# Performance work log

Measured on AMD Instinct MI355X. Metric: run time of the kernel, lower is better.

The kernel has to match this reference:

```python
import jax, jax.numpy as jnp
import numpy as np

NEG_INF = -jnp.inf


def setup_inputs() -> dict:
    key = jax.random.key(0)
    ks = jax.random.split(key, 8)
    B, Lq, Lk, D, H = 8, 2048, 2048, 256, 128
    queries = jax.random.normal(ks[0], (B, Lq, D), dtype=jnp.float32)
    keys = jax.random.normal(ks[1], (B, Lk, D), dtype=jnp.float32)
    values_1 = jax.random.normal(ks[2], (B, Lk, D), dtype=jnp.float32)
    values_2 = jax.random.normal(ks[3], (B, Lq, D), dtype=jnp.float32)
    values_1_mask = jax.random.randint(ks[4], (B, Lk), 0, 2).astype(bool)
    values_2_mask = jax.random.randint(ks[5], (B, Lq), 0, 2).astype(bool)
    # xavier_normal for Linear(D -> H): std = sqrt(2/(D+H))
    std = float(np.sqrt(2.0 / (D + H)))
    Wq = jax.random.normal(ks[6], (H, D), dtype=jnp.float32) * std
    Wk = jax.random.normal(ks[7], (H, D), dtype=jnp.float32) * std
    scaling = jnp.ones((1, H), dtype=jnp.float32)
    return {
        "queries": queries, "keys": keys,
        "values_1": values_1, "values_1_mask": values_1_mask,
        "values_2": values_2, "values_2_mask": values_2_mask,
        "Wq": Wq, "Wk": Wk, "scaling": scaling,
    }


def reference(queries, keys, values_1, values_1_mask, values_2, values_2_mask, Wq, Wk, scaling):
    # projections + relu (eval mode: dropout inactive)
    pq = jax.nn.relu(jnp.einsum("bqd,hd->bqh", queries, Wq))        # [B,Lq,H]
    pk = jax.nn.relu(jnp.einsum("bkd,hd->bkh", keys, Wk)) * scaling  # [B,Lk,H]
    scores = jnp.einsum("bqh,bkh->bqk", pq, pk)                      # [B,Lq,Lk]

    # branch 2: softmax over queries axis of scores^T, masked by values_2_mask [B,Lq]
    scores_T = jnp.where(values_2_mask[:, None, :], NEG_INF, jnp.swapaxes(scores, 1, 2))  # [B,Lk,Lq]
    alpha_2 = jax.nn.softmax(scores_T, axis=2)
    output_2 = jnp.einsum("bkq,bqd->bkd", alpha_2, values_2)         # [B,Lk,D]

    # branch 1: softmax over keys axis, masked by values_1_mask [B,Lk]
    scores_1 = jnp.where(values_1_mask[:, None, :], NEG_INF, scores)  # [B,Lq,Lk]
    alpha_1 = jax.nn.softmax(scores_1, axis=2)
    output = jnp.einsum("bqk,bkd->bqd", alpha_1, values_1)           # [B,Lq,D]

    return (output, output_2)
```

## Files before the change

kernel.cpp:

```cpp
#include <hip/hip_runtime.h>
#include <cstdint>
#include <math.h>

#define B 8
#define L 2048
#define D 256
#define H 128

typedef __attribute__((ext_vector_type(8))) _Float16 half8;
typedef __attribute__((ext_vector_type(4))) _Float16 half4t;
typedef __attribute__((ext_vector_type(4))) float f32x4;
typedef unsigned short ushort;
typedef unsigned int uint;


__global__ void prep_kernel(const void* __restrict__ raw0,
                            const void* __restrict__ raw1,
                            const float* __restrict__ Wq,
                            const float* __restrict__ Wk,
                            float* __restrict__ fb1,
                            float* __restrict__ fb2,
                            _Float16* __restrict__ Wf) {
    const int t = threadIdx.x;
    const int z = blockIdx.y;
    {
        const void* raw = z ? raw1 : raw0;
        float* outb = z ? fb2 : fb1;
        const uint* wd = (const uint*)raw;
        __shared__ int flag;
        if (t == 0) flag = 0;
        __syncthreads();
        if (wd[t] > 1u) flag = 1;
        __syncthreads();
        const int base = blockIdx.x * 1024;
        if (flag) {
            const uint8_t* by = (const uint8_t*)raw;
#pragma unroll
            for (int j = 0; j < 4; ++j) {
                int i = base + t + 256 * j;
                outb[i] = by[i] ? -INFINITY : 0.f;
            }
        } else {
#pragma unroll
            for (int j = 0; j < 4; ++j) {
                int i = base + t + 256 * j;
                outb[i] = wd[i] ? -INFINITY : 0.f;
            }
        }
    }
    {
        const float* Wsrc = z ? Wk : Wq;
        const int chunk = blockIdx.x * 256 + t;
        const int h = chunk >> 5;
        const int d0 = (chunk & 31) * 8;
        float4 v0 = *(const float4*)(Wsrc + (size_t)h * 256 + d0);
        float4 v1 = *(const float4*)(Wsrc + (size_t)h * 256 + d0 + 4);
        half8 hv;
        hv[0] = (_Float16)v0.x; hv[1] = (_Float16)v0.y;
        hv[2] = (_Float16)v0.z; hv[3] = (_Float16)v0.w;
        hv[4] = (_Float16)v1.x; hv[5] = (_Float16)v1.y;
        hv[6] = (_Float16)v1.z; hv[7] = (_Float16)v1.w;
        const int db = d0 >> 5, dq = (d0 >> 3) & 3;
        size_t off = (size_t)z * 32768 +
                     ((size_t)((h >> 4) * 8 + db)) * 512 + dq * 128 + (h & 15) * 8;
        *(half8*)(Wf + off) = hv;
    }
}

__launch_bounds__(256, 2)
__global__ void proj_mfma_kernel(const float* __restrict__ queries,
                                 const float* __restrict__ keys,
                                 const _Float16* __restrict__ Wf,
                                 const float* __restrict__ scaling,
                                 _Float16* __restrict__ pqo,
                                 _Float16* __restrict__ pko) {
    const int t = threadIdx.x;
    const int w = t >> 6;
    const int lane = t & 63;
    const int l15 = lane & 15;
    const int quad = lane >> 4;
    const int z = blockIdx.z;
    const int half = blockIdx.y;
    const int r0 = blockIdx.x * 64;
    const float* in = z ? keys : queries;
    _Float16* outp = z ? pko : pqo;

    __shared__ __attribute__((aligned(16))) _Float16 Wl[32 * 512];
    __shared__ __attribute__((aligned(16))) _Float16 Af[4][8 * 512];

    {
        const _Float16* wsrc = Wf + ((size_t)z * 64 + half * 32) * 512;
#pragma unroll
        for (int i = 0; i < 8; ++i) {
            const int f = w * 8 + i;
            __builtin_amdgcn_global_load_lds(
                (const __attribute__((address_space(1))) uint*)(wsrc + f * 512 + lane * 8),
                (__attribute__((address_space(3))) uint*)(Wl + f * 512 + lane * 8),
                16, 0, 0);
        }
    }
    {
#pragma unroll
        for (int j = 0; j < 16; ++j) {
            const int idx = t + 256 * j;
            const int row = idx >> 6;
            const int c4 = idx & 63;
            float4 v = *(const float4*)(in + ((size_t)(r0 + row)) * 256 + c4 * 4);
            half4t h4;
            h4[0] = (_Float16)v.x; h4[1] = (_Float16)v.y;
            h4[2] = (_Float16)v.z; h4[3] = (_Float16)v.w;
            const int rt = row >> 4, rl = row & 15;
            const int d0 = c4 * 4;
            const int db = d0 >> 5, dq = (d0 >> 3) & 3, e = d0 & 7;
            *(half4t*)(&Af[rt][db * 512 + dq * 128 + rl * 8 + e]) = h4;
        }
    }
    __syncthreads();

    half8 a[8];
#pragma unroll
    for (int db = 0; db < 8; ++db)
        a[db] = *(const half8*)(&Af[w][db * 512 + lane * 8]);

    f32x4 acc[4];
#pragma unroll
    for (int hti = 0; hti < 4; ++hti) acc[hti] = (f32x4){0.f, 0.f, 0.f, 0.f};
#pragma unroll
    for (int db = 0; db < 8; ++db)
#pragma unroll
        for (int hti = 0; hti < 4; ++hti) {
            half8 bfrag = *(const half8*)(Wl + (hti * 8 + db) * 512 + lane * 8);
            acc[hti] = __builtin_amdgcn_mfma_f32_16x16x32_f16(a[db], bfrag, acc[hti], 0, 0, 0);
        }

    _Float16* S = Af[w];
#pragma unroll
    for (int hti = 0; hti < 4; ++hti) {
        const int hl_ = hti * 16 + l15;
        const int hb = hl_ >> 5, hq = (hl_ >> 3) & 3, e = hl_ & 7;
        const float scl = z ? scaling[half * 64 + hl_] : 1.f;
#pragma unroll
        for (int r = 0; r < 4; ++r) {
            float v = fmaxf(acc[hti][r], 0.f) * scl;
            S[hb * 512 + hq * 128 + (quad * 4 + r) * 8 + e] = (_Float16)v;
        }
    }
    const size_t grow16 = (size_t)(r0 >> 4) + w;
    _Float16* gout = outp + (grow16 * 4 + half * 2) * 512;
#pragma unroll
    for (int hb = 0; hb < 2; ++hb) {
        half8 vv = *(const half8*)(S + hb * 512 + lane * 8);
        *(half8*)(gout + hb * 512 + lane * 8) = vv;
    }
}

__global__ void vtrans_kernel(const float* __restrict__ v1,
                              const float* __restrict__ v2,
                              _Float16* __restrict__ vt1,
                              _Float16* __restrict__ vt2) {
    const int t = threadIdx.x;
    const int zz = blockIdx.z;
    const int b = zz & 7;
    const int which = zz >> 3;
    const float* src = (which ? v2 : v1) + (size_t)b * L * D;
    _Float16* dst = which ? vt2 : vt1;
    const int k0 = blockIdx.x * 64;
    const int d0 = blockIdx.y * 64;
    __shared__ float lt[64][65];
#pragma unroll
    for (int p = 0; p < 4; ++p) {
        int kr = p * 16 + (t >> 4);
        float4 v = *(const float4*)(src + (size_t)(k0 + kr) * D + d0 + (t & 15) * 4);
        lt[(t & 15) * 4 + 0][kr] = v.x;
        lt[(t & 15) * 4 + 1][kr] = v.y;
        lt[(t & 15) * 4 + 2][kr] = v.z;
        lt[(t & 15) * 4 + 3][kr] = v.w;
    }
    __syncthreads();
    const int d = t & 63;
    const int kk = (t >> 6) & 1;
    const int qp = t >> 7;
    const size_t tile = ((size_t)b * L + k0) / 32 + kk;
    const int ct = (d0 + d) >> 4;
    _Float16* base = dst + (tile * 16 + ct) * 512 + (d & 15) * 8;
#pragma unroll
    for (int s = 0; s < 2; ++s) {
        const int qv = qp * 2 + s;
        const float* lr = &lt[d][kk * 32 + qv * 8];
        half8 hv;
#pragma unroll
        for (int e = 0; e < 8; ++e) hv[e] = (_Float16)lr[e];
        *(half8*)(base + qv * 128) = hv;
    }
}

__launch_bounds__(256, 3)
__global__ void flash_mfma_kernel(const _Float16* __restrict__ pq,
                                  const _Float16* __restrict__ pk,
                                  const float* __restrict__ fb1,
                                  const float* __restrict__ fb2,
                                  const _Float16* __restrict__ vt1,
                                  const _Float16* __restrict__ vt2,
                                  float* __restrict__ out) {
    const int t = threadIdx.x;
    const int w = t >> 6;
    const int lane = t & 63;
    const int l15 = lane & 15;
    const int quad = lane >> 4;
    const int bb = blockIdx.y;
    const int q0 = blockIdx.x * 64 + w * 16;

    const _Float16 *Qp, *Kp, *Vp;
    const float* fb;
    float* O;
    if (blockIdx.z == 0) { Qp = pq; Kp = pk; fb = fb1; Vp = vt1; O = out; }
    else                 { Qp = pk; Kp = pq; fb = fb2; Vp = vt2; O = out + (size_t)B * L * D; }

    __shared__ __attribute__((aligned(16))) _Float16 kv[2][24 * 512];
    __shared__ __attribute__((aligned(16))) _Float16 Pl[4][16][40];

    const size_t bL = (size_t)bb * L;

    half8 aq[4];
    {
        const _Float16* qb = Qp + (size_t)((bL + q0) >> 4) * 2048 + lane * 8;
#pragma unroll
        for (int hb = 0; hb < 4; ++hb) aq[hb] = *(const half8*)(qb + hb * 512);
    }

    f32x4 acc[16];
#pragma unroll
    for (int ct = 0; ct < 16; ++ct) acc[ct] = (f32x4){0.f, 0.f, 0.f, 0.f};
    float m_run[4], l_run[4];
#pragma unroll
    for (int r = 0; r < 4; ++r) { m_run[r] = -INFINITY; l_run[r] = 0.f; }

    auto stage = [&](int tile, int buf) {
        const size_t kk0 = bL + (size_t)tile * 32;
        _Float16* lb = kv[buf];
#pragma unroll
        for (int i = 0; i < 6; ++i) {
            const int c = w * 6 + i;
            const _Float16* g;
            if (c < 8)
                g = Kp + (size_t)(((kk0 >> 4) + (c >> 2)) * 4 + (c & 3)) * 512;
            else
                g = Vp + (size_t)((kk0 >> 5) * 16 + (c - 8)) * 512;
            __builtin_amdgcn_global_load_lds(
                (const __attribute__((address_space(1))) uint*)(g + lane * 8),
                (__attribute__((address_space(3))) uint*)(lb + c * 512),
                16, 0, 0);
        }
    };

    stage(0, 0);
    float nb0 = fb[bL + l15];
    float nb1 = fb[bL + 16 + l15];

    for (int it = 0; it < L / 32; ++it) {
        const int buf = it & 1;
        __syncthreads();
        if (it + 1 < L / 32) stage(it + 1, buf ^ 1);
        const float bias0 = nb0, bias1 = nb1;
        if (it + 1 < L / 32) {
            nb0 = fb[bL + (it + 1) * 32 + l15];
            nb1 = fb[bL + (it + 1) * 32 + 16 + l15];
        }

        const _Float16* kb = kv[buf];

        f32x4 s[2];
#pragma unroll
        for (int jt = 0; jt < 2; ++jt) {
            f32x4 sv = (f32x4){0.f, 0.f, 0.f, 0.f};
#pragma unroll
            for (int hb = 0; hb < 4; ++hb) {
                half8 bk = *(const half8*)(kb + (jt * 4 + hb) * 512 + lane * 8);
                sv = __builtin_amdgcn_mfma_f32_16x16x32_f16(aq[hb], bk, sv, 0, 0, 0);
            }
            s[jt] = sv;
        }
#pragma unroll
        for (int r = 0; r < 4; ++r) { s[0][r] += bias0; s[1][r] += bias1; }

        float al[4];
#pragma unroll
        for (int r = 0; r < 4; ++r) {
            float tm = fmaxf(s[0][r], s[1][r]);
            tm = fmaxf(tm, __shfl_xor(tm, 1));
            tm = fmaxf(tm, __shfl_xor(tm, 2));
            tm = fmaxf(tm, __shfl_xor(tm, 4));
            tm = fmaxf(tm, __shfl_xor(tm, 8));
            const float mn = fmaxf(m_run[r], tm);
            const float alpha = (m_run[r] == -INFINITY) ? 0.f : __expf(m_run[r] - mn);
            const float safe = (mn == -INFINITY) ? 0.f : mn;
            _Float16 p0 = (_Float16)__expf(s[0][r] - safe);
            _Float16 p1 = (_Float16)__expf(s[1][r] - safe);
            Pl[w][quad * 4 + r][l15] = p0;
            Pl[w][quad * 4 + r][16 + l15] = p1;
            float ps = (float)p0 + (float)p1;
            ps += __shfl_xor(ps, 1);
            ps += __shfl_xor(ps, 2);
            ps += __shfl_xor(ps, 4);
            ps += __shfl_xor(ps, 8);
            m_run[r] = mn;
            l_run[r] = l_run[r] * alpha + ps;
            al[r] = alpha;
        }

        const bool need = (al[0] != 1.f) | (al[1] != 1.f) | (al[2] != 1.f) | (al[3] != 1.f);
        if (__any(need)) {
#pragma unroll
            for (int ct = 0; ct < 16; ++ct)
#pragma unroll
                for (int r = 0; r < 4; ++r) acc[ct][r] *= al[r];
        }

        half8 pa = *(const half8*)&Pl[w][l15][quad * 8];
#pragma unroll
        for (int ct = 0; ct < 16; ++ct) {
            half8 bv = *(const half8*)(kb + (8 + ct) * 512 + lane * 8);
            acc[ct] = __builtin_amdgcn_mfma_f32_16x16x32_f16(pa, bv, acc[ct], 0, 0, 0);
        }
    }

    float inv[4];
#pragma unroll
    for (int r = 0; r < 4; ++r)
        inv[r] = (l_run[r] > 0.f) ? (1.f / l_run[r]) : 0.f;
#pragma unroll
    for (int r = 0; r < 4; ++r) {
        float* orow = O + (bL + q0 + quad * 4 + r) * (size_t)D + l15;
#pragma unroll
        for (int ct = 0; ct < 16; ++ct)
            orow[ct * 16] = acc[ct][r] * inv[r];
    }
}

extern "C" void kernel_launch(void* const* d_in, const int* in_sizes, int n_in,
                              void* d_out, int out_size, void* d_ws, size_t ws_size,
                              hipStream_t stream) {
    const float* queries  = (const float*)d_in[0];
    const float* keys     = (const float*)d_in[1];
    const float* values_1 = (const float*)d_in[2];
    const void*  v1_mask  = d_in[3];
    const float* values_2 = (const float*)d_in[4];
    const void*  v2_mask  = d_in[5];
    const float* Wq       = (const float*)d_in[6];
    const float* Wk       = (const float*)d_in[7];
    const float* scaling  = (const float*)d_in[8];
    float* out = (float*)d_out;

    _Float16* pqw = (_Float16*)d_ws;
    _Float16* pkw = pqw + (size_t)B * L * H;
    _Float16* vt1 = pkw + (size_t)B * L * H;
    _Float16* vt2 = vt1 + (size_t)B * L * D;
    float* fb1 = (float*)(vt2 + (size_t)B * L * D);
    float* fb2 = fb1 + B * L;
    _Float16* Wf = (_Float16*)(fb2 + B * L);

    prep_kernel<<<dim3(16, 2), 256, 0, stream>>>(
        v1_mask, v2_mask, Wq, Wk, fb1, fb2, Wf);
    proj_mfma_kernel<<<dim3(B * L / 64, 2, 2), 256, 0, stream>>>(
        queries, keys, Wf, scaling, pqw, pkw);
    vtrans_kernel<<<dim3(L / 64, D / 64, B * 2), 256, 0, stream>>>(
        values_1, values_2, vt1, vt2);
    flash_mfma_kernel<<<dim3(L / 64, B, 2), 256, 0, stream>>>(
        pqw, pkw, fb1, fb2, vt1, vt2, out);
}
```

Baseline: 256.0 us.

## Compute scores once, share them across both softmax branches with precomputed row maxima

Replaces the fused flash kernel, which computed QK^T twice (once per branch), with a score kernel that computes each score tile once. It stores the tile in fp16 relative to a per-tile max and records per-row and per-column tile maxima. A second kernel reduces these maxima into exact row maxes up front, then exponentiates the stored scores and runs the PV MFMA without online rescaling. This halves the QK matmul work and removes the running-max correction, but adds a 64 MB fp16 score buffer written and read through global memory. The transposed branch also reads scores through LDS with strided accesses.

```diff
diff --git a/kernel.cpp b/kernel.cpp
--- a/kernel.cpp
+++ b/kernel.cpp
@@ -194,146 +194,237 @@
     }
 }
 
+__launch_bounds__(256)
+__global__ void score_kernel(const _Float16* __restrict__ pq,
+                             const _Float16* __restrict__ pk,
+                             const float* __restrict__ fb1,
+                             const float* __restrict__ fb2,
+                             _Float16* __restrict__ Sb,
+                             float* __restrict__ tmax1,
+                             float* __restrict__ tmax2,
+                             float* __restrict__ mmax) {
+    const int t = threadIdx.x;
+    const int w = t >> 6;
+    const int lane = t & 63;
+    const int l15 = lane & 15;
+    const int quad = lane >> 4;
+    const int bb = blockIdx.z;
+    const int k0 = blockIdx.x * 64;
+    const int q0 = blockIdx.y * 64;
+    const size_t bL = (size_t)bb * L;
+    const int qt16 = (q0 >> 4) + w;
+
+    half8 aq[4];
+    {
+        const _Float16* qb = pq + ((bL + q0 + w * 16) >> 4) * 2048 + lane * 8;
+#pragma unroll
+        for (int hb = 0; hb < 4; ++hb) aq[hb] = *(const half8*)(qb + hb * 512);
+    }
+
+    f32x4 s[4];
+#pragma unroll
+    for (int jt = 0; jt < 4; ++jt) {
+        const _Float16* kb = pk + ((bL + k0 + jt * 16) >> 4) * 2048 + lane * 8;
+        f32x4 sv = (f32x4){0.f, 0.f, 0.f, 0.f};
+#pragma unroll
+        for (int hb = 0; hb < 4; ++hb) {
+            half8 bk = *(const half8*)(kb + hb * 512);
+            sv = __builtin_amdgcn_mfma_f32_16x16x32_f16(aq[hb], bk, sv, 0, 0, 0);
+        }
+        s[jt] = sv;
+    }
+
+    float b1j[4];
+#pragma unroll
+    for (int jt = 0; jt < 4; ++jt) b1j[jt] = fb1[bL + k0 + jt * 16 + l15];
+    float4 b2v = *(const float4*)(fb2 + bL + q0 + w * 16 + quad * 4);
+    float b2r[4] = {b2v.x, b2v.y, b2v.z, b2v.w};
+
+#pragma unroll
+    for (int r = 0; r < 4; ++r) {
+        float m1 = -INFINITY;
+#pragma unroll
+        for (int jt = 0; jt < 4; ++jt) m1 = fmaxf(m1, s[jt][r] + b1j[jt]);
+        m1 = fmaxf(m1, __shfl_xor(m1, 1));
+        m1 = fmaxf(m1, __shfl_xor(m1, 2));
+        m1 = fmaxf(m1, __shfl_xor(m1, 4));
+        m1 = fmaxf(m1, __shfl_xor(m1, 8));
+        if (l15 == 0)
+            tmax1[(bL + q0 + w * 16 + quad * 4 + r) * 32 + blockIdx.x] = m1;
+    }
+
+#pragma unroll
+    for (int jt = 0; jt < 4; ++jt) {
+        float m2 = -INFINITY, mm = -INFINITY;
+#pragma unroll
+        for (int r = 0; r < 4; ++r) {
+            m2 = fmaxf(m2, s[jt][r] + b2r[r]);
+            mm = fmaxf(mm, s[jt][r]);
+        }
+        m2 = fmaxf(m2, __shfl_xor(m2, 16));
+        m2 = fmaxf(m2, __shfl_xor(m2, 32));
+        if (quad == 0)
+            tmax2[(bL + k0 + jt * 16 + l15) * 128 + qt16] = m2;
+        mm = fmaxf(mm, __shfl_xor(mm, 1));
+        mm = fmaxf(mm, __shfl_xor(mm, 2));
+        mm = fmaxf(mm, __shfl_xor(mm, 4));
+        mm = fmaxf(mm, __shfl_xor(mm, 8));
+        mm = fmaxf(mm, __shfl_xor(mm, 16));
+        mm = fmaxf(mm, __shfl_xor(mm, 32));
+        const size_t mti = ((size_t)bb * 128 + qt16) * 128 + (k0 >> 4) + jt;
+        if (lane == 0) mmax[mti] = mm;
+        _Float16* sp = Sb + mti * 256 + l15;
+#pragma unroll
+        for (int r = 0; r < 4; ++r)
+            sp[(quad * 4 + r) * 16] = (_Float16)(s[jt][r] - mm);
+    }
+}
+
 __launch_bounds__(256, 3)
-__global__ void flash_mfma_kernel(const _Float16* __restrict__ pq,
-                                  const _Float16* __restrict__ pk,
-                                  const float* __restrict__ fb1,
-                                  const float* __restrict__ fb2,
-                                  const _Float16* __restrict__ vt1,
-                                  const _Float16* __restrict__ vt2,
-                                  float* __restrict__ out) {
+__global__ void attn_pv_kernel(const _Float16* __restrict__ Sb,
+                               const float* __restrict__ fb1,
+                               const float* __restrict__ fb2,
+                               const float* __restrict__ tmax1,
+                               const float* __restrict__ tmax2,
+                               const float* __restrict__ mmax,
+                               const _Float16* __restrict__ vt1,
+                               const _Float16* __restrict__ vt2,
+                               float* __restrict__ out) {
     const int t = threadIdx.x;
     const int w = t >> 6;
     const int lane = t & 63;
     const int l15 = lane & 15;
     const int quad = lane >> 4;
     const int bb = blockIdx.y;
-    const int q0 = blockIdx.x * 64 + w * 16;
-
-    const _Float16 *Qp, *Kp, *Vp;
-    const float* fb;
-    float* O;
-    if (blockIdx.z == 0) { Qp = pq; Kp = pk; fb = fb1; Vp = vt1; O = out; }
-    else                 { Qp = pk; Kp = pq; fb = fb2; Vp = vt2; O = out + (size_t)B * L * D; }
-
-    __shared__ __attribute__((aligned(16))) _Float16 kv[2][24 * 512];
-    __shared__ __attribute__((aligned(16))) _Float16 Pl[4][16][40];
-
+    const int z = blockIdx.z;
+    const int r0 = blockIdx.x * 64;
     const size_t bL = (size_t)bb * L;
 
-    half8 aq[4];
-    {
-        const _Float16* qb = Qp + (size_t)((bL + q0) >> 4) * 2048 + lane * 8;
-#pragma unroll
-        for (int hb = 0; hb < 4; ++hb) aq[hb] = *(const half8*)(qb + hb * 512);
+    const _Float16* Vp = z ? vt2 : vt1;
+    const float* fbb = (z ? fb2 : fb1) + bL;
+    float* O = out + (z ? (size_t)B * L * D : 0);
+
+    __shared__ __attribute__((aligned(16))) _Float16 kv[2][16 * 512];
+    __shared__ __attribute__((aligned(16))) _Float16 sst[2][4 * 1056];
+    __shared__ float mred[64][4];
+
+    {
+        const int row = t >> 2, part = t & 3;
+        float mv = -INFINITY;
+        if (z == 0) {
+            const float4* p4 = (const float4*)(tmax1 + ((bL + r0 + row) << 5)) + part * 2;
+#pragma unroll
+            for (int i = 0; i < 2; ++i) {
+                float4 v = p4[i];
+                mv = fmaxf(mv, fmaxf(fmaxf(v.x, v.y), fmaxf(v.z, v.w)));
+            }
+        } else {
+            const float4* p4 = (const float4*)(tmax2 + ((bL + r0 + row) << 7)) + part * 8;
+#pragma unroll
+            for (int i = 0; i < 8; ++i) {
+                float4 v = p4[i];
+                mv = fmaxf(mv, fmaxf(fmaxf(v.x, v.y), fmaxf(v.z, v.w)));
+            }
+        }
+        mred[row][part] = mv;
+    }
+
+    auto stage = [&](int it, int buf) {
+        const _Float16* vb = Vp + ((bL + it * 32) >> 5) * (size_t)(16 * 512);
+#pragma unroll
+        for (int i = 0; i < 4; ++i) {
+            const int c = w * 4 + i;
+            __builtin_amdgcn_global_load_lds(
+                (const __attribute__((address_space(1))) uint*)(vb + c * 512 + lane * 8),
+                (__attribute__((address_space(3))) uint*)(&kv[buf][c * 512] + lane * 8),
+                16, 0, 0);
+        }
+        if (z) {
+            const _Float16* ssrc = Sb +
+                (((size_t)bb * 128 + it * 2 + (w >> 1)) * 128 + (r0 >> 4) + (w & 1) * 2) * 256;
+            __builtin_amdgcn_global_load_lds(
+                (const __attribute__((address_space(1))) uint*)(ssrc + lane * 8),
+                (__attribute__((address_space(3))) uint*)(&sst[buf][w * 1056] + lane * 8),
+                16, 0, 0);
+        }
+    };
+
+    stage(0, 0);
+    __syncthreads();
+
+    float mreg;
+    {
+        const int row = w * 16 + l15;
+        mreg = fmaxf(fmaxf(mred[row][0], mred[row][1]),
+                     fmaxf(mred[row][2], mred[row][3]));
+        mreg = fmaxf(mreg, -1e30f);
     }
 
     f32x4 acc[16];
 #pragma unroll
     for (int ct = 0; ct < 16; ++ct) acc[ct] = (f32x4){0.f, 0.f, 0.f, 0.f};
-    float m_run[4], l_run[4];
-#pragma unroll
-    for (int r = 0; r < 4; ++r) { m_run[r] = -INFINITY; l_run[r] = 0.f; }
-
-    auto stage = [&](int tile, int buf) {
-        const size_t kk0 = bL + (size_t)tile * 32;
-        _Float16* lb = kv[buf];
-#pragma unroll
-        for (int i = 0; i < 6; ++i) {
-            const int c = w * 6 + i;
-            const _Float16* g;
-            if (c < 8)
-                g = Kp + (size_t)(((kk0 >> 4) + (c >> 2)) * 4 + (c & 3)) * 512;
-            else
-                g = Vp + (size_t)((kk0 >> 5) * 16 + (c - 8)) * 512;
-            __builtin_amdgcn_global_load_lds(
-                (const __attribute__((address_space(1))) uint*)(g + lane * 8),
-                (__attribute__((address_space(3))) uint*)(lb + c * 512),
-                16, 0, 0);
-        }
-    };
-
-    stage(0, 0);
-    float nb0 = fb[bL + l15];
-    float nb1 = fb[bL + 16 + l15];
-
-    for (int it = 0; it < L / 32; ++it) {
+    float lsum = 0.f;
+
+    for (int it = 0; it < 64; ++it) {
         const int buf = it & 1;
-        __syncthreads();
-        if (it + 1 < L / 32) stage(it + 1, buf ^ 1);
-        const float bias0 = nb0, bias1 = nb1;
-        if (it + 1 < L / 32) {
-            nb0 = fb[bL + (it + 1) * 32 + l15];
-            nb1 = fb[bL + (it + 1) * 32 + 16 + l15];
-        }
-
+        if (it) __syncthreads();
+        if (it + 1 < 64) stage(it + 1, buf ^ 1);
+
+        float c;
+        {
+            const size_t mmidx = z
+                ? (((size_t)bb * 128 + it * 2 + (quad >> 1)) * 128 + (r0 >> 4) + w)
+                : (((size_t)bb * 128 + (r0 >> 4) + w) * 128 + it * 2 + (quad >> 1));
+            c = mmax[mmidx] - mreg;
+        }
+        float bj[8];
+        {
+            const float4* bp = (const float4*)(fbb + it * 32 + quad * 8);
+            float4 b0 = bp[0], b1 = bp[1];
+            bj[0] = b0.x; bj[1] = b0.y; bj[2] = b0.z; bj[3] = b0.w;
+            bj[4] = b1.x; bj[5] = b1.y; bj[6] = b1.z; bj[7] = b1.w;
+        }
+        float pj[8];
+        if (z == 0) {
+            const _Float16* sp = Sb +
+                (((size_t)bb * 128 + (r0 >> 4) + w) * 128 + it * 2 + (quad >> 1)) * 256 +
+                l15 * 16 + (quad & 1) * 8;
+            half8 sv = *(const half8*)sp;
+#pragma unroll
+            for (int j = 0; j < 8; ++j) pj[j] = (float)sv[j];
+        } else {
+            const _Float16* sl = &sst[buf][((quad >> 1) * 2 + (w >> 1)) * 1056 +
+                                           (w & 1) * 256 + l15];
+#pragma unroll
+            for (int j = 0; j < 8; ++j)
+                pj[j] = (float)sl[((quad & 1) * 8 + j) * 16];
+        }
+        half8 pa;
+#pragma unroll
+        for (int j = 0; j < 8; ++j) {
+            float p = __expf(pj[j] + c + bj[j]);
+            pa[j] = (_Float16)p;
+            lsum += (float)pa[j];
+        }
         const _Float16* kb = kv[buf];
-
-        f32x4 s[2];
-#pragma unroll
-        for (int jt = 0; jt < 2; ++jt) {
-            f32x4 sv = (f32x4){0.f, 0.f, 0.f, 0.f};
-#pragma unroll
-            for (int hb = 0; hb < 4; ++hb) {
-                half8 bk = *(const half8*)(kb + (jt * 4 + hb) * 512 + lane * 8);
-                sv = __builtin_amdgcn_mfma_f32_16x16x32_f16(aq[hb], bk, sv, 0, 0, 0);
-            }
-            s[jt] = sv;
-        }
-#pragma unroll
-        for (int r = 0; r < 4; ++r) { s[0][r] += bias0; s[1][r] += bias1; }
-
-        float al[4];
-#pragma unroll
-        for (int r = 0; r < 4; ++r) {
-            float tm = fmaxf(s[0][r], s[1][r]);
-            tm = fmaxf(tm, __shfl_xor(tm, 1));
-            tm = fmaxf(tm, __shfl_xor(tm, 2));
-            tm = fmaxf(tm, __shfl_xor(tm, 4));
-            tm = fmaxf(tm, __shfl_xor(tm, 8));
-            const float mn = fmaxf(m_run[r], tm);
-            const float alpha = (m_run[r] == -INFINITY) ? 0.f : __expf(m_run[r] - mn);
-            const float safe = (mn == -INFINITY) ? 0.f : mn;
-            _Float16 p0 = (_Float16)__expf(s[0][r] - safe);
-            _Float16 p1 = (_Float16)__expf(s[1][r] - safe);
-            Pl[w][quad * 4 + r][l15] = p0;
-            Pl[w][quad * 4 + r][16 + l15] = p1;
-            float ps = (float)p0 + (float)p1;
-            ps += __shfl_xor(ps, 1);
-            ps += __shfl_xor(ps, 2);
-            ps += __shfl_xor(ps, 4);
-            ps += __shfl_xor(ps, 8);
-            m_run[r] = mn;
-            l_run[r] = l_run[r] * alpha + ps;
-            al[r] = alpha;
-        }
-
-        const bool need = (al[0] != 1.f) | (al[1] != 1.f) | (al[2] != 1.f) | (al[3] != 1.f);
-        if (__any(need)) {
-#pragma unroll
-            for (int ct = 0; ct < 16; ++ct)
-#pragma unroll
-                for (int r = 0; r < 4; ++r) acc[ct][r] *= al[r];
-        }
-
-        half8 pa = *(const half8*)&Pl[w][l15][quad * 8];
 #pragma unroll
         for (int ct = 0; ct < 16; ++ct) {
-            half8 bv = *(const half8*)(kb + (8 + ct) * 512 + lane * 8);
+            half8 bv = *(const half8*)(kb + ct * 512 + lane * 8);
             acc[ct] = __builtin_amdgcn_mfma_f32_16x16x32_f16(pa, bv, acc[ct], 0, 0, 0);
         }
     }
 
-    float inv[4];
-#pragma unroll
-    for (int r = 0; r < 4; ++r)
-        inv[r] = (l_run[r] > 0.f) ? (1.f / l_run[r]) : 0.f;
+    lsum += __shfl_xor(lsum, 16);
+    lsum += __shfl_xor(lsum, 32);
+    float inv = (lsum > 0.f) ? (1.f / lsum) : 0.f;
+
 #pragma unroll
     for (int r = 0; r < 4; ++r) {
-        float* orow = O + (bL + q0 + quad * 4 + r) * (size_t)D + l15;
+        const float invr = __shfl(inv, quad * 4 + r);
+        float* orow = O + (bL + r0 + w * 16 + quad * 4 + r) * (size_t)D + l15;
 #pragma unroll
         for (int ct = 0; ct < 16; ++ct)
-            orow[ct * 16] = acc[ct][r] * inv[r];
+            orow[ct * 16] = acc[ct][r] * invr;
     }
 }
 
@@ -355,9 +446,13 @@
     _Float16* pkw = pqw + (size_t)B * L * H;
     _Float16* vt1 = pkw + (size_t)B * L * H;
     _Float16* vt2 = vt1 + (size_t)B * L * D;
-    float* fb1 = (float*)(vt2 + (size_t)B * L * D);
-    float* fb2 = fb1 + B * L;
-    _Float16* Wf = (_Float16*)(fb2 + B * L);
+    _Float16* Sb  = vt2 + (size_t)B * L * D;
+    float* fb1   = (float*)(Sb + (size_t)B * 128 * 128 * 256);
+    float* fb2   = fb1 + B * L;
+    float* tmax1 = fb2 + B * L;
+    float* tmax2 = tmax1 + (size_t)B * L * 32;
+    float* mmaxp = tmax2 + (size_t)B * L * 128;
+    _Float16* Wf = (_Float16*)(mmaxp + (size_t)B * 128 * 128);
 
     prep_kernel<<<dim3(16, 2), 256, 0, stream>>>(
         v1_mask, v2_mask, Wq, Wk, fb1, fb2, Wf);
@@ -365,6 +460,8 @@
         queries, keys, Wf, scaling, pqw, pkw);
     vtrans_kernel<<<dim3(L / 64, D / 64, B * 2), 256, 0, stream>>>(
         values_1, values_2, vt1, vt2);
-    flash_mfma_kernel<<<dim3(L / 64, B, 2), 256, 0, stream>>>(
-        pqw, pkw, fb1, fb2, vt1, vt2, out);
-}
+    score_kernel<<<dim3(L / 64, L / 64, B), 256, 0, stream>>>(
+        pqw, pkw, fb1, fb2, Sb, tmax1, tmax2, mmaxp);
+    attn_pv_kernel<<<dim3(L / 64, B, 2), 256, 0, stream>>>(
+        Sb, fb1, fb2, tmax1, tmax2, mmaxp, vt1, vt2, out);
+}
```

Result: faster. 243.0 us (-5.1%).
